# Optimization experiments

Hardware: AMD Instinct MI355X
Metric: run time of the kernel (lower is better)

Reference implementation:

```python
import jax, jax.numpy as jnp
import numpy as np

B, L = 512, 61440
E_MAX = 128          # max events per window (padded)
THRESHOLD = 0.5      # prob -> binary threshold
IOU_THR = 0.2        # IoU match threshold
LEN_THR = 128        # int(freq*time) = int(256*0.5)


def setup_inputs() -> dict:
    key = jax.random.key(0)
    k1, k2 = jax.random.split(key)
    # block-structured signals -> realistic long, sparse events
    out_blocks = jax.random.uniform(k1, (B, L // 256), dtype=jnp.float32)
    output = jnp.repeat(out_blocks, 256, axis=1)            # [B, L] probs
    tgt_blocks = (jax.random.uniform(k2, (B, L // 512)) > 0.75).astype(jnp.float32)
    target = jnp.repeat(tgt_blocks, 512, axis=1)            # [B, L] binary
    return {"output": output, "target": target}


def _filter_short(b):
    # zero out runs of ones shorter than LEN_THR (ProcessingPostEvent)
    starts = jnp.concatenate([b[:1], ((b[1:] - b[:-1]) == 1).astype(b.dtype)])
    run_id = jnp.cumsum(starts)                              # [L]
    run_len = jax.ops.segment_sum(b, run_id, num_segments=L + 1)
    return b * (run_len[run_id] >= LEN_THR).astype(b.dtype)


def _events(b):
    # binary_to_array: [start, end) pairs, padded to E_MAX with [L, L]
    padded = jnp.concatenate([jnp.zeros(1, b.dtype), b, jnp.zeros(1, b.dtype)])
    d = padded[1:] - padded[:-1]                             # [L+1]
    pos = jnp.arange(L + 1)
    starts = jnp.sort(jnp.where(d == 1, pos, L + 1))[:E_MAX]
    ends = jnp.sort(jnp.where(d == -1, pos, L + 1))[:E_MAX]
    starts = jnp.minimum(starts, L)
    ends = jnp.minimum(ends, L)
    n = (d == 1).sum()
    return starts, ends, n


def _best_match(iou):
    # iou: [E_MAX, E_MAX], invalid entries = -1
    max_col = iou.max(0); idx_col = iou.argmax(0)            # best output row per target col
    max_row = iou.max(1); idx_row = iou.argmax(1)            # best target col per output row
    ar = jnp.arange(E_MAX)
    mutual_row = (idx_col[idx_row] == ar) & (max_row >= IOU_THR)   # [E] rows in mutual match
    mutual_col = (idx_row[idx_col] == ar) & (max_col >= IOU_THR)   # [E] cols in mutual match
    row_one = (~mutual_row) & (max_row >= IOU_THR)
    col_one = (~mutual_col) & (max_col >= IOU_THR)
    onehot_row = (ar[None, :] == idx_row[:, None])           # bm[i, idx_row[i]]
    onehot_col = (ar[:, None] == idx_col[None, :])           # bm[idx_col[j], j]
    ones_m = (onehot_row & row_one[:, None]) | (onehot_col & col_one[None, :])
    kill = mutual_row[:, None] | mutual_col[None, :]         # rows/cols of mutual matches zeroed
    ones_m = ones_m & (~kill)
    tp = mutual_row.sum()                                    # count of '2' marks
    return tp, ones_m


def _per_batch(out_prob, tgt):
    b_out = _filter_short((out_prob >= THRESHOLD).astype(jnp.int32))
    b_tgt = (tgt != 0).astype(jnp.int32)
    s_o, e_o, n_out = _events(b_out)
    s_t, e_t, n_tgt = _events(b_tgt)
    inter = jnp.clip(jnp.minimum(e_o[:, None], e_t[None, :])
                     - jnp.maximum(s_o[:, None], s_t[None, :]), 0)
    la = (e_o - s_o)[:, None]
    lb = (e_t - s_t)[None, :]
    den = jnp.maximum(la + lb - inter, 1)
    valid = (jnp.arange(E_MAX) < n_out)[:, None] & (jnp.arange(E_MAX) < n_tgt)[None, :]
    iou = jnp.where(valid, inter.astype(jnp.float32) / den.astype(jnp.float32), -1.0)
    tp1, ones_m = _best_match(iou)
    # second pass on positions marked '1' (iou elsewhere zeroed in original)
    tp2, _ = _best_match(jnp.where(ones_m, iou, -1.0))
    tp = tp1 + tp2
    t_empty = n_tgt == 0
    o_empty = (~t_empty) & (n_out == 0)
    tp_b = jnp.where(t_empty | o_empty, 0, tp)
    # note: faithful to original (adds output count to FN when target empty, etc.)
    fn_b = jnp.where(t_empty, n_out, jnp.where(o_empty, 0, n_tgt - tp))
    fp_b = jnp.where(t_empty, 0, jnp.where(o_empty, n_tgt, n_out - tp))
    return tp_b, fn_b, fp_b


def reference(output, target):
    tp, fn, fp = jax.vmap(_per_batch)(output, target)
    TP = tp.sum().astype(jnp.float32)
    FN = fn.sum().astype(jnp.float32)
    FP = fp.sum().astype(jnp.float32)
    recall = jnp.where(TP + FN == 0, 0.0, TP / jnp.maximum(TP + FN, 1.0))
    precision = jnp.where(TP + FP == 0, 0.0, TP / jnp.maximum(TP + FP, 1.0))
    f1 = jnp.where(precision + recall == 0, 0.0,
                   2.0 * precision * recall / jnp.maximum(precision + recall, 1e-30))
    return recall, precision, f1
```

## Files before the change

### kernel.cpp

```cpp
#include <hip/hip_runtime.h>

typedef unsigned long long ull;

#define L_LEN 61440
#define NBATCH 512
#define EMAX 128
#define RUNBUF 128
#define NWORDS 960
#define NPADW 1080
#define PADW(w) ((w) + ((w) >> 3))
#define NTHREADS 1024
#define IOU_THRESH 0.2f
#define LEN_THRESH 128
#define PADPK 0xF000F000u

__device__ __forceinline__ unsigned int mask16_ge(float4 a, float4 b, float4 c, float4 d, float thr) {
    unsigned int m = 0;
    m |= (a.x >= thr) ? 0x0001u : 0u; m |= (a.y >= thr) ? 0x0002u : 0u;
    m |= (a.z >= thr) ? 0x0004u : 0u; m |= (a.w >= thr) ? 0x0008u : 0u;
    m |= (b.x >= thr) ? 0x0010u : 0u; m |= (b.y >= thr) ? 0x0020u : 0u;
    m |= (b.z >= thr) ? 0x0040u : 0u; m |= (b.w >= thr) ? 0x0080u : 0u;
    m |= (c.x >= thr) ? 0x0100u : 0u; m |= (c.y >= thr) ? 0x0200u : 0u;
    m |= (c.z >= thr) ? 0x0400u : 0u; m |= (c.w >= thr) ? 0x0800u : 0u;
    m |= (d.x >= thr) ? 0x1000u : 0u; m |= (d.y >= thr) ? 0x2000u : 0u;
    m |= (d.z >= thr) ? 0x4000u : 0u; m |= (d.w >= thr) ? 0x8000u : 0u;
    return m;
}

__device__ __forceinline__ unsigned int mask16_ne0(float4 a, float4 b, float4 c, float4 d) {
    unsigned int m = 0;
    m |= (a.x != 0.0f) ? 0x0001u : 0u; m |= (a.y != 0.0f) ? 0x0002u : 0u;
    m |= (a.z != 0.0f) ? 0x0004u : 0u; m |= (a.w != 0.0f) ? 0x0008u : 0u;
    m |= (b.x != 0.0f) ? 0x0010u : 0u; m |= (b.y != 0.0f) ? 0x0020u : 0u;
    m |= (b.z != 0.0f) ? 0x0040u : 0u; m |= (b.w != 0.0f) ? 0x0080u : 0u;
    m |= (c.x != 0.0f) ? 0x0100u : 0u; m |= (c.y != 0.0f) ? 0x0200u : 0u;
    m |= (c.z != 0.0f) ? 0x0400u : 0u; m |= (c.w != 0.0f) ? 0x0800u : 0u;
    m |= (d.x != 0.0f) ? 0x1000u : 0u; m |= (d.y != 0.0f) ? 0x2000u : 0u;
    m |= (d.z != 0.0f) ? 0x4000u : 0u; m |= (d.w != 0.0f) ? 0x8000u : 0u;
    return m;
}

__device__ __forceinline__ float iou_pk(unsigned int pk, int ms, int me, int ml) {
    int s = (int)(pk & 0xffffu), e = (int)(pk >> 16);
    int lo = me < e ? me : e;
    int hi = ms > s ? ms : s;
    int inter = lo - hi; if (inter < 0) inter = 0;
    int den = ml + (e - s) - inter; if (den < 1) den = 1;
    return (float)inter / (float)den;
}

__global__ __launch_bounds__(NTHREADS) void event_f1_kernel(
        const float* __restrict__ outp, const float* __restrict__ tgtp,
        int* __restrict__ per_row) {
    __shared__ ull bm[2][NPADW];
    __shared__ int runs_s[2][RUNBUF], runs_e[2][RUNBUF];
    __shared__ int wtot_s[16], wtot_e[16];
    __shared__ __align__(16) unsigned int pse_o[EMAX], pse_t[EMAX];
    __shared__ int idxr[EMAX], idxc[EMAX];
    __shared__ __align__(16) unsigned int rowfl[EMAX], colfl[EMAX];
    __shared__ int n_out_s, n_tgt_s, ftot0, tp_sh;

    const int tid = threadIdx.x;
    const int lane = tid & 63;
    const int wid = tid >> 6;
    const int row = blockIdx.x;

    const float* op = outp + (size_t)row * L_LEN;
    const float* tg = tgtp + (size_t)row * L_LEN;

    if (tid == 0) tp_sh = 0;

    unsigned short* bmo16 = (unsigned short*)bm[0];
    unsigned short* bmt16 = (unsigned short*)bm[1];
    #pragma unroll 1
    for (int it = 0; it < 4; ++it) {
        if (it == 3 && tid >= 768) break;
        const float4* po = (const float4*)(op + it * 16384 + tid * 16);
        const float4* pt = (const float4*)(tg + it * 16384 + tid * 16);
        float4 a0 = po[0], a1 = po[1], a2 = po[2], a3 = po[3];
        float4 b0 = pt[0], b1 = pt[1], b2 = pt[2], b3 = pt[3];
        unsigned int mo = mask16_ge(a0, a1, a2, a3, 0.5f);
        unsigned int mt = mask16_ne0(b0, b1, b2, b3);
        unsigned int u = it * 1024 + tid;
        unsigned int pu = u + ((u >> 5) << 2);
        bmo16[pu] = (unsigned short)mo;
        bmt16[pu] = (unsigned short)mt;
    }
    __syncthreads();

    const int group = tid >> 8;
    const int g = group & 1;
    const int gtid = tid & 255;
    const ull* bmp = bm[g];
    const int w0 = gtid * 4;
    const bool act = (tid < 512) && (gtid < 240);

    ull swm0 = 0, swm1 = 0, swm2 = 0, swm3 = 0;
    ull ewm0 = 0, ewm1 = 0, ewm2 = 0, ewm3 = 0;
    int cs = 0, ce = 0;
    if (act) {
        ull wm1 = (w0 > 0) ? bmp[PADW(w0 - 1)] : 0ull;
        int p0 = PADW(w0);
        ull a = bmp[p0], b = bmp[p0 + 1], c = bmp[p0 + 2], d = bmp[p0 + 3];
        ull wp4 = (w0 + 4 < NWORDS) ? bmp[PADW(w0 + 4)] : 0ull;
        swm0 = a & ~((a << 1) | (wm1 >> 63)); ewm0 = a & ~((a >> 1) | (b << 63));
        swm1 = b & ~((b << 1) | (a >> 63));   ewm1 = b & ~((b >> 1) | (c << 63));
        swm2 = c & ~((c << 1) | (b >> 63));   ewm2 = c & ~((c >> 1) | (d << 63));
        swm3 = d & ~((d << 1) | (c >> 63));   ewm3 = d & ~((d >> 1) | (wp4 << 63));
        cs = __popcll(swm0) + __popcll(swm1) + __popcll(swm2) + __popcll(swm3);
        ce = __popcll(ewm0) + __popcll(ewm1) + __popcll(ewm2) + __popcll(ewm3);
    }
    int incl_s = cs, incl_e = ce;
    #pragma unroll
    for (int d = 1; d < 64; d <<= 1) {
        int us = __shfl_up(incl_s, d, 64);
        int ue = __shfl_up(incl_e, d, 64);
        if (lane >= d) { incl_s += us; incl_e += ue; }
    }
    if (lane == 63) { wtot_s[wid] = incl_s; wtot_e[wid] = incl_e; }
    __syncthreads();
    int off_s = incl_s - cs, off_e = incl_e - ce;
    if (act) {
        for (int wv = (g << 2); wv < wid; ++wv) { off_s += wtot_s[wv]; off_e += wtot_e[wv]; }
        ull m; int base;
        m = swm0; base = w0 * 64;
        while (m) { int z = __builtin_ctzll(m); if (off_s < RUNBUF) runs_s[g][off_s] = base + z; ++off_s; m &= m - 1; }
        m = swm1; base += 64;
        while (m) { int z = __builtin_ctzll(m); if (off_s < RUNBUF) runs_s[g][off_s] = base + z; ++off_s; m &= m - 1; }
        m = swm2; base += 64;
        while (m) { int z = __builtin_ctzll(m); if (off_s < RUNBUF) runs_s[g][off_s] = base + z; ++off_s; m &= m - 1; }
        m = swm3; base += 64;
        while (m) { int z = __builtin_ctzll(m); if (off_s < RUNBUF) runs_s[g][off_s] = base + z; ++off_s; m &= m - 1; }
        m = ewm0; base = w0 * 64;
        while (m) { int z = __builtin_ctzll(m); if (off_e < RUNBUF) runs_e[g][off_e] = base + z + 1; ++off_e; m &= m - 1; }
        m = ewm1; base += 64;
        while (m) { int z = __builtin_ctzll(m); if (off_e < RUNBUF) runs_e[g][off_e] = base + z + 1; ++off_e; m &= m - 1; }
        m = ewm2; base += 64;
        while (m) { int z = __builtin_ctzll(m); if (off_e < RUNBUF) runs_e[g][off_e] = base + z + 1; ++off_e; m &= m - 1; }
        m = ewm3; base += 64;
        while (m) { int z = __builtin_ctzll(m); if (off_e < RUNBUF) runs_e[g][off_e] = base + z + 1; ++off_e; m &= m - 1; }
    }
    __syncthreads();

    const int nro = wtot_s[0] + wtot_s[1] + wtot_s[2] + wtot_s[3];
    const int nrt = wtot_s[4] + wtot_s[5] + wtot_s[6] + wtot_s[7];

    int keep = 0, fs = 0, fe = 0, fincl = 0;
    if (tid < 128) {
        int lim = nro < RUNBUF ? nro : RUNBUF;
        if (tid < lim) { fs = runs_s[0][tid]; fe = runs_e[0][tid]; keep = (fe - fs) >= LEN_THRESH ? 1 : 0; }
        fincl = keep;
        #pragma unroll
        for (int d = 1; d < 64; d <<= 1) {
            int u = __shfl_up(fincl, d, 64);
            if (lane >= d) fincl += u;
        }
        if (tid == 63) ftot0 = fincl;
    } else if (tid < 256) {
        int k = tid - 128;
        int mc = nrt < EMAX ? nrt : EMAX;
        pse_t[k] = (k < mc) ? ((unsigned)runs_s[1][k] | ((unsigned)runs_e[1][k] << 16)) : PADPK;
        if (k == 0) n_tgt_s = nrt;
    }
    __syncthreads();
    if (tid < 128) {
        int off = fincl - keep + (tid >= 64 ? ftot0 : 0);
        if (keep && off < EMAX) pse_o[off] = (unsigned)fs | ((unsigned)fe << 16);
        if (tid == 127) n_out_s = ftot0 + fincl;
    }
    __syncthreads();
    {
        int mcl = n_out_s < EMAX ? n_out_s : EMAX;
        if (tid < 128 && tid >= mcl) pse_o[tid] = PADPK;
    }
    __syncthreads();

    int ntc = n_tgt_s < EMAX ? n_tgt_s : EMAX;
    int noc = n_out_s < EMAX ? n_out_s : EMAX;
    const int nt4 = (ntc + 3) & ~3;
    const int no4 = (noc + 3) & ~3;

    unsigned mypk = PADPK;
    if (tid < 128) mypk = pse_o[tid];
    else if (tid < 256) mypk = pse_t[tid - 128];
    const int my_s = (int)(mypk & 0xffffu);
    const int my_e = (int)(mypk >> 16);
    const int my_len = my_e - my_s;

    float best = -2.0f; int bi = 0;
    if (tid < 128) {
        for (int j = 0; j < nt4; j += 4) {
            uint4 pk = *(const uint4*)&pse_t[j];
            float v0 = iou_pk(pk.x, my_s, my_e, my_len);
            float v1 = iou_pk(pk.y, my_s, my_e, my_len);
            float v2 = iou_pk(pk.z, my_s, my_e, my_len);
            float v3 = iou_pk(pk.w, my_s, my_e, my_len);
            if (v0 > best) { best = v0; bi = j; }
            if (v1 > best) { best = v1; bi = j + 1; }
            if (v2 > best) { best = v2; bi = j + 2; }
            if (v3 > best) { best = v3; bi = j + 3; }
        }
        idxr[tid] = bi;
    } else if (tid < 256) {
        for (int i = 0; i < no4; i += 4) {
            uint4 pk = *(const uint4*)&pse_o[i];
            float v0 = iou_pk(pk.x, my_s, my_e, my_len);
            float v1 = iou_pk(pk.y, my_s, my_e, my_len);
            float v2 = iou_pk(pk.z, my_s, my_e, my_len);
            float v3 = iou_pk(pk.w, my_s, my_e, my_len);
            if (v0 > best) { best = v0; bi = i; }
            if (v1 > best) { best = v1; bi = i + 1; }
            if (v2 > best) { best = v2; bi = i + 2; }
            if (v3 > best) { best = v3; bi = i + 3; }
        }
        idxc[tid - 128] = bi;
    }
    __syncthreads();

    bool mm = false;
    if (tid < 128) mm = (idxc[bi] == tid) && (best >= IOU_THRESH);
    else if (tid < 256) mm = (idxr[bi] == tid - 128) && (best >= IOU_THRESH);
    if (tid < 128) {
        ull bb = __ballot(mm);
        if (lane == 0) atomicAdd(&tp_sh, (int)__popcll(bb));
    }
    __syncthreads();

    const int bi0 = bi;
    const bool m0 = mm;
    const bool one0 = (!mm) && (best >= IOU_THRESH);
    if (tid < 128)      rowfl[tid] = (unsigned)bi0 | (one0 ? 0x100u : 0u) | (m0 ? 0x200u : 0u);
    else if (tid < 256) colfl[tid - 128] = (unsigned)bi0 | (one0 ? 0x100u : 0u) | (m0 ? 0x200u : 0u);
    __syncthreads();

    best = -2.0f; bi = 0;
    if (tid < 128) {
        const int i = tid;
        for (int j = 0; j < nt4; j += 4) {
            uint4 pk = *(const uint4*)&pse_t[j];
            uint4 fl = *(const uint4*)&colfl[j];
            bool om0 = (((j + 0 == bi0) && one0) || ((i == (int)(fl.x & 0xffu)) && (fl.x & 0x100u))) && !m0 && !(fl.x & 0x200u);
            bool om1 = (((j + 1 == bi0) && one0) || ((i == (int)(fl.y & 0xffu)) && (fl.y & 0x100u))) && !m0 && !(fl.y & 0x200u);
            bool om2 = (((j + 2 == bi0) && one0) || ((i == (int)(fl.z & 0xffu)) && (fl.z & 0x100u))) && !m0 && !(fl.z & 0x200u);
            bool om3 = (((j + 3 == bi0) && one0) || ((i == (int)(fl.w & 0xffu)) && (fl.w & 0x100u))) && !m0 && !(fl.w & 0x200u);
            float v0 = om0 ? iou_pk(pk.x, my_s, my_e, my_len) : -1.0f;
            float v1 = om1 ? iou_pk(pk.y, my_s, my_e, my_len) : -1.0f;
            float v2 = om2 ? iou_pk(pk.z, my_s, my_e, my_len) : -1.0f;
            float v3 = om3 ? iou_pk(pk.w, my_s, my_e, my_len) : -1.0f;
            if (v0 > best) { best = v0; bi = j; }
            if (v1 > best) { best = v1; bi = j + 1; }
            if (v2 > best) { best = v2; bi = j + 2; }
            if (v3 > best) { best = v3; bi = j + 3; }
        }
        idxr[tid] = bi;
    } else if (tid < 256) {
        const int j = tid - 128;
        for (int i = 0; i < no4; i += 4) {
            uint4 pk = *(const uint4*)&pse_o[i];
            uint4 fl = *(const uint4*)&rowfl[i];
            bool om0 = (((j == (int)(fl.x & 0xffu)) && (fl.x & 0x100u)) || ((i + 0 == bi0) && one0)) && !(fl.x & 0x200u) && !m0;
            bool om1 = (((j == (int)(fl.y & 0xffu)) && (fl.y & 0x100u)) || ((i + 1 == bi0) && one0)) && !(fl.y & 0x200u) && !m0;
            bool om2 = (((j == (int)(fl.z & 0xffu)) && (fl.z & 0x100u)) || ((i + 2 == bi0) && one0)) && !(fl.z & 0x200u) && !m0;
            bool om3 = (((j == (int)(fl.w & 0xffu)) && (fl.w & 0x100u)) || ((i + 3 == bi0) && one0)) && !(fl.w & 0x200u) && !m0;
            float v0 = om0 ? iou_pk(pk.x, my_s, my_e, my_len) : -1.0f;
            float v1 = om1 ? iou_pk(pk.y, my_s, my_e, my_len) : -1.0f;
            float v2 = om2 ? iou_pk(pk.z, my_s, my_e, my_len) : -1.0f;
            float v3 = om3 ? iou_pk(pk.w, my_s, my_e, my_len) : -1.0f;
            if (v0 > best) { best = v0; bi = i; }
            if (v1 > best) { best = v1; bi = i + 1; }
            if (v2 > best) { best = v2; bi = i + 2; }
            if (v3 > best) { best = v3; bi = i + 3; }
        }
        idxc[tid - 128] = bi;
    }
    __syncthreads();

    mm = false;
    if (tid < 128) mm = (idxc[bi] == tid) && (best >= IOU_THRESH);
    else if (tid < 256) mm = (idxr[bi] == tid - 128) && (best >= IOU_THRESH);
    if (tid < 128) {
        ull bb = __ballot(mm);
        if (lane == 0) atomicAdd(&tp_sh, (int)__popcll(bb));
    }
    __syncthreads();

    if (tid == 0) {
        int n_out = n_out_s, n_tgt = n_tgt_s, tp = tp_sh;
        int tpb, fnb, fpb;
        if (n_tgt == 0)      { tpb = 0;  fnb = n_out;      fpb = 0; }
        else if (n_out == 0) { tpb = 0;  fnb = 0;          fpb = n_tgt; }
        else                 { tpb = tp; fnb = n_tgt - tp; fpb = n_out - tp; }
        per_row[row * 3 + 0] = tpb;
        per_row[row * 3 + 1] = fnb;
        per_row[row * 3 + 2] = fpb;
    }
}

__global__ __launch_bounds__(512) void finalize_kernel(const int* __restrict__ per_row,
                                                       float* __restrict__ out) {
    __shared__ int sm[3][8];
    const int tid = threadIdx.x;
    const int lane = tid & 63;
    const int wid = tid >> 6;
    int tp = per_row[tid * 3 + 0];
    int fn = per_row[tid * 3 + 1];
    int fp = per_row[tid * 3 + 2];
    #pragma unroll
    for (int d = 32; d > 0; d >>= 1) {
        tp += __shfl_down(tp, d, 64);
        fn += __shfl_down(fn, d, 64);
        fp += __shfl_down(fp, d, 64);
    }
    if (lane == 0) { sm[0][wid] = tp; sm[1][wid] = fn; sm[2][wid] = fp; }
    __syncthreads();
    if (tid == 0) {
        int TPi = 0, FNi = 0, FPi = 0;
        #pragma unroll
        for (int w = 0; w < 8; ++w) { TPi += sm[0][w]; FNi += sm[1][w]; FPi += sm[2][w]; }
        float TP = (float)TPi, FN = (float)FNi, FP = (float)FPi;
        float rd = TP + FN;
        float recall = (rd == 0.0f) ? 0.0f : TP / fmaxf(rd, 1.0f);
        float pd = TP + FP;
        float precision = (pd == 0.0f) ? 0.0f : TP / fmaxf(pd, 1.0f);
        float s = precision + recall;
        float f1 = (s == 0.0f) ? 0.0f : 2.0f * precision * recall / fmaxf(s, 1e-30f);
        out[0] = recall; out[1] = precision; out[2] = f1;
    }
}

extern "C" void kernel_launch(void* const* d_in, const int* in_sizes, int n_in,
                              void* d_out, int out_size, void* d_ws, size_t ws_size,
                              hipStream_t stream) {
    const float* outp = (const float*)d_in[0];
    const float* tgtp = (const float*)d_in[1];
    float* res = (float*)d_out;
    int* per_row = (int*)d_ws;

    event_f1_kernel<<<NBATCH, NTHREADS, 0, stream>>>(outp, tgtp, per_row);
    finalize_kernel<<<1, 512, 0, stream>>>(per_row, res);
}
```

Before: 57.49 us.

## Split thresholding into separate wide mask kernel, shrink match kernel block

```diff
diff --git a/kernel.cpp b/kernel.cpp
--- a/kernel.cpp
+++ b/kernel.cpp
@@ -9,10 +9,13 @@
 #define NWORDS 960
 #define NPADW 1080
 #define PADW(w) ((w) + ((w) >> 3))
-#define NTHREADS 1024
 #define IOU_THRESH 0.2f
 #define LEN_THRESH 128
 #define PADPK 0xF000F000u
+
+#define BM_WORDS_PER_ROW 960
+#define BM_USHORT_PER_ROW 3840
+#define PER_ROW_OFF (2u * NBATCH * BM_WORDS_PER_ROW * 8u)
 
 __device__ __forceinline__ unsigned int mask16_ge(float4 a, float4 b, float4 c, float4 d, float thr) {
     unsigned int m = 0;
@@ -49,12 +52,37 @@
     return (float)inter / (float)den;
 }
 
-__global__ __launch_bounds__(NTHREADS) void event_f1_kernel(
+__global__ __launch_bounds__(256) void mask_kernel(
         const float* __restrict__ outp, const float* __restrict__ tgtp,
+        unsigned short* __restrict__ bmo_g, unsigned short* __restrict__ bmt_g) {
+    const int bid = blockIdx.x;
+    const int row = bid / 5;
+    const int chunk = bid % 5;
+    const int tid = threadIdx.x;
+
+    const float* op = outp + (size_t)row * L_LEN + chunk * 12288;
+    const float* tg = tgtp + (size_t)row * L_LEN + chunk * 12288;
+    const int obase = row * BM_USHORT_PER_ROW + chunk * 768;
+
+    #pragma unroll
+    for (int it = 0; it < 3; ++it) {
+        const float4* po = (const float4*)(op + it * 4096 + tid * 16);
+        const float4* pt = (const float4*)(tg + it * 4096 + tid * 16);
+        float4 a0 = po[0], a1 = po[1], a2 = po[2], a3 = po[3];
+        float4 b0 = pt[0], b1 = pt[1], b2 = pt[2], b3 = pt[3];
+        unsigned int mo = mask16_ge(a0, a1, a2, a3, 0.5f);
+        unsigned int mt = mask16_ne0(b0, b1, b2, b3);
+        bmo_g[obase + it * 256 + tid] = (unsigned short)mo;
+        bmt_g[obase + it * 256 + tid] = (unsigned short)mt;
+    }
+}
+
+__global__ __launch_bounds__(512) void match_kernel(
+        const ull* __restrict__ bmo_u, const ull* __restrict__ bmt_u,
         int* __restrict__ per_row) {
     __shared__ ull bm[2][NPADW];
     __shared__ int runs_s[2][RUNBUF], runs_e[2][RUNBUF];
-    __shared__ int wtot_s[16], wtot_e[16];
+    __shared__ int wtot_s[8], wtot_e[8];
     __shared__ __align__(16) unsigned int pse_o[EMAX], pse_t[EMAX];
     __shared__ int idxr[EMAX], idxc[EMAX];
     __shared__ __align__(16) unsigned int rowfl[EMAX], colfl[EMAX];
@@ -65,48 +93,32 @@
     const int wid = tid >> 6;
     const int row = blockIdx.x;
 
-    const float* op = outp + (size_t)row * L_LEN;
-    const float* tg = tgtp + (size_t)row * L_LEN;
-
     if (tid == 0) tp_sh = 0;
 
-    unsigned short* bmo16 = (unsigned short*)bm[0];
-    unsigned short* bmt16 = (unsigned short*)bm[1];
-    #pragma unroll 1
-    for (int it = 0; it < 4; ++it) {
-        if (it == 3 && tid >= 768) break;
-        const float4* po = (const float4*)(op + it * 16384 + tid * 16);
-        const float4* pt = (const float4*)(tg + it * 16384 + tid * 16);
-        float4 a0 = po[0], a1 = po[1], a2 = po[2], a3 = po[3];
-        float4 b0 = pt[0], b1 = pt[1], b2 = pt[2], b3 = pt[3];
-        unsigned int mo = mask16_ge(a0, a1, a2, a3, 0.5f);
-        unsigned int mt = mask16_ne0(b0, b1, b2, b3);
-        unsigned int u = it * 1024 + tid;
-        unsigned int pu = u + ((u >> 5) << 2);
-        bmo16[pu] = (unsigned short)mo;
-        bmt16[pu] = (unsigned short)mt;
-    }
-    __syncthreads();
-
-    const int group = tid >> 8;
-    const int g = group & 1;
+    const int g = tid >> 8;
     const int gtid = tid & 255;
-    const ull* bmp = bm[g];
     const int w0 = gtid * 4;
-    const bool act = (tid < 512) && (gtid < 240);
+    const bool act = (gtid < 240);
+    const ull* bsrc = (g == 0 ? bmo_u : bmt_u) + (size_t)row * BM_WORDS_PER_ROW;
+
+    ull a = 0, b = 0, c = 0, dd = 0;
+    if (act) {
+        a = bsrc[w0]; b = bsrc[w0 + 1]; c = bsrc[w0 + 2]; dd = bsrc[w0 + 3];
+        int p0 = PADW(w0);
+        bm[g][p0] = a; bm[g][p0 + 1] = b; bm[g][p0 + 2] = c; bm[g][p0 + 3] = dd;
+    }
+    __syncthreads();
 
     ull swm0 = 0, swm1 = 0, swm2 = 0, swm3 = 0;
     ull ewm0 = 0, ewm1 = 0, ewm2 = 0, ewm3 = 0;
     int cs = 0, ce = 0;
     if (act) {
-        ull wm1 = (w0 > 0) ? bmp[PADW(w0 - 1)] : 0ull;
-        int p0 = PADW(w0);
-        ull a = bmp[p0], b = bmp[p0 + 1], c = bmp[p0 + 2], d = bmp[p0 + 3];
-        ull wp4 = (w0 + 4 < NWORDS) ? bmp[PADW(w0 + 4)] : 0ull;
+        ull wm1 = (w0 > 0) ? bm[g][PADW(w0 - 1)] : 0ull;
+        ull wp4 = (w0 + 4 < NWORDS) ? bm[g][PADW(w0 + 4)] : 0ull;
         swm0 = a & ~((a << 1) | (wm1 >> 63)); ewm0 = a & ~((a >> 1) | (b << 63));
         swm1 = b & ~((b << 1) | (a >> 63));   ewm1 = b & ~((b >> 1) | (c << 63));
-        swm2 = c & ~((c << 1) | (b >> 63));   ewm2 = c & ~((c >> 1) | (d << 63));
-        swm3 = d & ~((d << 1) | (c >> 63));   ewm3 = d & ~((d >> 1) | (wp4 << 63));
+        swm2 = c & ~((c << 1) | (b >> 63));   ewm2 = c & ~((c >> 1) | (dd << 63));
+        swm3 = dd & ~((dd << 1) | (c >> 63)); ewm3 = dd & ~((dd >> 1) | (wp4 << 63));
         cs = __popcll(swm0) + __popcll(swm1) + __popcll(swm2) + __popcll(swm3);
         ce = __popcll(ewm0) + __popcll(ewm1) + __popcll(ewm2) + __popcll(ewm3);
     }
@@ -334,8 +346,13 @@
     const float* outp = (const float*)d_in[0];
     const float* tgtp = (const float*)d_in[1];
     float* res = (float*)d_out;
-    int* per_row = (int*)d_ws;
-
-    event_f1_kernel<<<NBATCH, NTHREADS, 0, stream>>>(outp, tgtp, per_row);
+
+    char* ws = (char*)d_ws;
+    unsigned short* bmo_g = (unsigned short*)ws;
+    unsigned short* bmt_g = (unsigned short*)(ws + (size_t)NBATCH * BM_WORDS_PER_ROW * 8);
+    int* per_row = (int*)(ws + PER_ROW_OFF);
+
+    mask_kernel<<<NBATCH * 5, 256, 0, stream>>>(outp, tgtp, bmo_g, bmt_g);
+    match_kernel<<<NBATCH, 512, 0, stream>>>((const ull*)bmo_g, (const ull*)bmt_g, per_row);
     finalize_kernel<<<1, 512, 0, stream>>>(per_row, res);
 }
```

Result: slower. 62.40 us (+8.5%).

## Shrink block to 768 threads and software-pipeline the bitmask load loop

Applied to the files above, without the earlier changes.

```diff
diff --git a/kernel.cpp b/kernel.cpp
--- a/kernel.cpp
+++ b/kernel.cpp
@@ -9,7 +9,7 @@
 #define NWORDS 960
 #define NPADW 1080
 #define PADW(w) ((w) + ((w) >> 3))
-#define NTHREADS 1024
+#define NTHREADS 768
 #define IOU_THRESH 0.2f
 #define LEN_THRESH 128
 #define PADPK 0xF000F000u
@@ -49,7 +49,21 @@
     return (float)inter / (float)den;
 }
 
-__global__ __launch_bounds__(NTHREADS) void event_f1_kernel(
+#define LOAD8(A0,A1,A2,A3,B0,B1,B2,B3, IT) { \
+    const float4* po_ = (const float4*)(op + (IT) * 12288 + tid * 16); \
+    const float4* pt_ = (const float4*)(tg + (IT) * 12288 + tid * 16); \
+    A0 = po_[0]; A1 = po_[1]; A2 = po_[2]; A3 = po_[3]; \
+    B0 = pt_[0]; B1 = pt_[1]; B2 = pt_[2]; B3 = pt_[3]; }
+
+#define PROC(IT, A0,A1,A2,A3,B0,B1,B2,B3) { \
+    unsigned int mo_ = mask16_ge(A0, A1, A2, A3, 0.5f); \
+    unsigned int mt_ = mask16_ne0(B0, B1, B2, B3); \
+    unsigned int u_ = (IT) * NTHREADS + tid; \
+    unsigned int pu_ = u_ + ((u_ >> 5) << 2); \
+    bmo16[pu_] = (unsigned short)mo_; \
+    bmt16[pu_] = (unsigned short)mt_; }
+
+__global__ __launch_bounds__(NTHREADS, 6) void event_f1_kernel(
         const float* __restrict__ outp, const float* __restrict__ tgtp,
         int* __restrict__ per_row) {
     __shared__ ull bm[2][NPADW];
@@ -72,19 +86,19 @@
 
     unsigned short* bmo16 = (unsigned short*)bm[0];
     unsigned short* bmt16 = (unsigned short*)bm[1];
-    #pragma unroll 1
-    for (int it = 0; it < 4; ++it) {
-        if (it == 3 && tid >= 768) break;
-        const float4* po = (const float4*)(op + it * 16384 + tid * 16);
-        const float4* pt = (const float4*)(tg + it * 16384 + tid * 16);
-        float4 a0 = po[0], a1 = po[1], a2 = po[2], a3 = po[3];
-        float4 b0 = pt[0], b1 = pt[1], b2 = pt[2], b3 = pt[3];
-        unsigned int mo = mask16_ge(a0, a1, a2, a3, 0.5f);
-        unsigned int mt = mask16_ne0(b0, b1, b2, b3);
-        unsigned int u = it * 1024 + tid;
-        unsigned int pu = u + ((u >> 5) << 2);
-        bmo16[pu] = (unsigned short)mo;
-        bmt16[pu] = (unsigned short)mt;
+    {
+        float4 a0, a1, a2, a3, b0, b1, b2, b3;
+        float4 c0, c1, c2, c3, d0, d1, d2, d3;
+        LOAD8(a0, a1, a2, a3, b0, b1, b2, b3, 0);
+        LOAD8(c0, c1, c2, c3, d0, d1, d2, d3, 1);
+        PROC(0, a0, a1, a2, a3, b0, b1, b2, b3);
+        LOAD8(a0, a1, a2, a3, b0, b1, b2, b3, 2);
+        PROC(1, c0, c1, c2, c3, d0, d1, d2, d3);
+        LOAD8(c0, c1, c2, c3, d0, d1, d2, d3, 3);
+        PROC(2, a0, a1, a2, a3, b0, b1, b2, b3);
+        LOAD8(a0, a1, a2, a3, b0, b1, b2, b3, 4);
+        PROC(3, c0, c1, c2, c3, d0, d1, d2, d3);
+        PROC(4, a0, a1, a2, a3, b0, b1, b2, b3);
     }
     __syncthreads();
 
```

Result: faster. 55.99 us (-2.6%).
